# Performance work log

Hardware: AMD Instinct MI355X
Metric: run time of the kernel (lower is better)

The kernel has to match this reference:

```python
import jax, jax.numpy as jnp
import numpy as np

B, T, C, H = 2, 2048, 1024, 16
D = C // H  # head dim = 64

def setup_inputs() -> dict:
    key = jax.random.key(0)
    k1, k2, k3 = jax.random.split(key, 3)
    x = jax.random.normal(k1, (B, T, C), dtype=jnp.float32)
    w_attn = jax.random.normal(k2, (C, 3 * C), dtype=jnp.float32) * (1.0 / np.sqrt(C))
    w_proj = jax.random.normal(k3, (C, C), dtype=jnp.float32) * (1.0 / np.sqrt(C))
    return {"x": x, "w_attn": w_attn, "w_proj": w_proj}

def reference(x, w_attn, w_proj):
    # qkv projection: [B,T,3C]
    qkv = jnp.einsum('btc,cd->btd', x, w_attn)
    q, k, v = jnp.split(qkv, 3, axis=-1)
    # reshape to [B,H,T,D]
    q = q.reshape(B, T, H, D).transpose(0, 2, 1, 3)
    k = k.reshape(B, T, H, D).transpose(0, 2, 1, 3)
    v = v.reshape(B, T, H, D).transpose(0, 2, 1, 3)
    scale = 1.0 / jnp.sqrt(jnp.asarray(D, dtype=q.dtype))
    att = jnp.einsum('bhqd,bhkd->bhqk', q, k) * scale  # [B,H,T,T]
    att = jax.nn.softmax(att, axis=-1)
    y = jnp.einsum('bhqk,bhkd->bhqd', att, v)  # [B,H,T,D]
    y = y.transpose(0, 2, 1, 3).reshape(B, T, C)
    return jnp.einsum('btc,cd->btd', y, w_proj)
```

## Files before the change

### kernel.cpp

```cpp
#include <hip/hip_runtime.h>
#include <hip/hip_bf16.h>


typedef unsigned short u16;
using bf16x8 = __attribute__((ext_vector_type(8))) short;
using f32x4  = __attribute__((ext_vector_type(4))) float;

#define T_SEQ 2048
#define CDIM  1024

#define QSCALE 0.18033688011112042f

#if __has_builtin(__builtin_amdgcn_exp2f)
#define EXP2(x) __builtin_amdgcn_exp2f(x)
#else
#define EXP2(x) __expf((x) * 0.6931471805599453f)
#endif

__device__ inline u16 f2bf(float f) {
  __hip_bfloat16 h = __float2bfloat16(f);
  return *reinterpret_cast<u16*>(&h);
}
__device__ inline unsigned pk2bf(float a, float b) {
  return (unsigned)f2bf(a) | ((unsigned)f2bf(b) << 16);
}

__device__ inline void gload_lds16(const u16* g, u16* l) {
  __builtin_amdgcn_global_load_lds((const __attribute__((address_space(1))) void*)g,
                                   (__attribute__((address_space(3))) void*)l, 16, 0, 0);
}

__device__ inline int swz128(int r, int c) {
  return (((r << 7) + (c << 1)) ^ ((r & 7) << 4)) >> 1;
}

__global__ __launch_bounds__(256) void conv_bf16_kernel(const float* __restrict__ in,
                                                        u16* __restrict__ out, int n4) {
  int idx = blockIdx.x * 256 + threadIdx.x;
  if (idx >= n4) return;
  float4 v = reinterpret_cast<const float4*>(in)[idx];
  ushort4 o;
  o.x = f2bf(v.x); o.y = f2bf(v.y); o.z = f2bf(v.z); o.w = f2bf(v.w);
  reinterpret_cast<ushort4*>(out)[idx] = o;
}

__global__ __launch_bounds__(256) void transp_conv_kernel(const float* __restrict__ in,
                                                          u16* __restrict__ out, int R, int N,
                                                          int scale_rows, float scale) {
  __shared__ float tile[32][33];
  int nbx = N >> 5;
  int bx = blockIdx.x % nbx, by = blockIdx.x / nbx;
  int tx = threadIdx.x & 31, ty = threadIdx.x >> 5;
#pragma unroll
  for (int rr = ty; rr < 32; rr += 8)
    tile[rr][tx] = in[(long)(by * 32 + rr) * N + bx * 32 + tx];
  __syncthreads();
#pragma unroll
  for (int rr = ty; rr < 32; rr += 8) {
    float s = (bx * 32 + rr) < scale_rows ? scale : 1.0f;
    out[(long)(bx * 32 + rr) * R + by * 32 + tx] = f2bf(tile[tx][rr] * s);
  }
}

template <int MODE, int BN>
__global__ __launch_bounds__(256) void gemm_bt_kernel(const u16* __restrict__ A,
                                                      const u16* __restrict__ Bt,
                                                      void* __restrict__ C,
                                                      u16* __restrict__ vT,
                                                      int N, int K) {
  constexpr int NJ = BN / 32;
  constexpr int WN = BN / 2;
  __shared__ u16 As[2][128 * 32];
  __shared__ u16 Bs[2][BN * 32];
  const int tid = threadIdx.x;
  const int lane = tid & 63, wid = tid >> 6;
  const int l16 = lane & 15, lh = lane >> 4;
  const int wm = wid >> 1, wn = wid & 1;
  const int tm = blockIdx.x & 31;
  const int tn = blockIdx.x >> 5;

  f32x4 acc[4][NJ];
#pragma unroll
  for (int i = 0; i < 4; ++i)
#pragma unroll
    for (int j = 0; j < NJ; ++j)
      acc[i][j] = f32x4{0.f, 0.f, 0.f, 0.f};

  const long aRow = (long)(tm * 128 + wid * 16 + (lane >> 2)) * K + (lane & 3) * 8;
  const long bRow = (long)(tn * BN + wid * 16 + (lane >> 2)) * K + (lane & 3) * 8;
  const long rstep = (long)64 * K;
  const int ldsOff = wid * 512;

  gload_lds16(A + aRow, As[0] + ldsOff);
  gload_lds16(A + aRow + rstep, As[0] + ldsOff + 2048);
  gload_lds16(Bt + bRow, Bs[0] + ldsOff);
  if (BN == 128) gload_lds16(Bt + bRow + rstep, Bs[0] + ldsOff + 2048);
  __syncthreads();

  int cur = 0;
  for (int k0 = 0; k0 < K; k0 += 32) {
    if (k0 + 32 < K) {
      gload_lds16(A + aRow + k0 + 32, As[cur ^ 1] + ldsOff);
      gload_lds16(A + aRow + rstep + k0 + 32, As[cur ^ 1] + ldsOff + 2048);
      gload_lds16(Bt + bRow + k0 + 32, Bs[cur ^ 1] + ldsOff);
      if (BN == 128) gload_lds16(Bt + bRow + rstep + k0 + 32, Bs[cur ^ 1] + ldsOff + 2048);
    }
    bf16x8 af[4], bfr[NJ];
#pragma unroll
    for (int i = 0; i < 4; ++i)
      af[i] = *reinterpret_cast<const bf16x8*>(&As[cur][(wm * 64 + i * 16 + l16) * 32 + lh * 8]);
#pragma unroll
    for (int j = 0; j < NJ; ++j)
      bfr[j] = *reinterpret_cast<const bf16x8*>(&Bs[cur][(wn * WN + j * 16 + l16) * 32 + lh * 8]);
#pragma unroll
    for (int i = 0; i < 4; ++i)
#pragma unroll
      for (int j = 0; j < NJ; ++j)
        acc[i][j] = __builtin_amdgcn_mfma_f32_16x16x32_bf16(af[i], bfr[j], acc[i][j], 0, 0, 0);
    __syncthreads();
    cur ^= 1;
  }

  if (MODE == 2 && tn >= 16) {
    const int bsel = tm >> 4;
    const int t0 = (tm & 15) * 128 + wm * 64 + lh * 4;
#pragma unroll
    for (int i = 0; i < 4; ++i) {
#pragma unroll
      for (int j = 0; j < NJ; ++j) {
        const int h = 2 * (tn - 16) + wn;
        const int d = j * 16 + l16;
        u16* dst = vT + (long)((bsel * 16 + h) * 64 + d) * T_SEQ + t0 + i * 16;
        uint2 w2;
        w2.x = pk2bf(acc[i][j][0], acc[i][j][1]);
        w2.y = pk2bf(acc[i][j][2], acc[i][j][3]);
        *reinterpret_cast<uint2*>(dst) = w2;
      }
    }
    return;
  }

#pragma unroll
  for (int i = 0; i < 4; ++i) {
#pragma unroll
    for (int j = 0; j < NJ; ++j) {
#pragma unroll
      for (int r = 0; r < 4; ++r) {
        long row = tm * 128 + wm * 64 + i * 16 + lh * 4 + r;
        long col = tn * BN + wn * WN + j * 16 + l16;
        if (MODE == 1)
          reinterpret_cast<float*>(C)[row * N + col] = acc[i][j][r];
        else
          reinterpret_cast<u16*>(C)[row * N + col] = f2bf(acc[i][j][r]);
      }
    }
  }
}

__global__ __launch_bounds__(256) void vtrans_kernel(const u16* __restrict__ qkv,
                                                     u16* __restrict__ vT) {
  __shared__ u16 Ts[64 * 64];
  const int tid = threadIdx.x;
  const int bid = blockIdx.x;
  const int tt = bid & 31, bh = bid >> 5;
  const int b = bh >> 4, h = bh & 15;
  const int sr = tid >> 2, sc = (tid & 3) * 16;
  const u16* src = qkv + (long)(b * T_SEQ + tt * 64 + sr) * 3072 + 2 * CDIM + h * 64 + sc;
  uint4 v0 = *reinterpret_cast<const uint4*>(src);
  uint4 v1 = *reinterpret_cast<const uint4*>(src + 8);
  *reinterpret_cast<uint4*>(&Ts[swz128(sr, sc)]) = v0;
  *reinterpret_cast<uint4*>(&Ts[swz128(sr, sc + 8)]) = v1;
  __syncthreads();
  union { uint4 u[2]; u16 s[16]; } o;
#pragma unroll
  for (int i = 0; i < 16; ++i) o.s[i] = Ts[swz128(sc + i, sr)];
  u16* dst = vT + (long)(bh * 64 + sr) * T_SEQ + tt * 64 + sc;
  reinterpret_cast<uint4*>(dst)[0] = o.u[0];
  reinterpret_cast<uint4*>(dst)[1] = o.u[1];
}

__global__ __launch_bounds__(256) void attn_kernel(const u16* __restrict__ qkv,
                                                   const u16* __restrict__ vT,
                                                   u16* __restrict__ y) {
  __shared__ u16 Qs[64 * 64];
  __shared__ u16 Ks[64 * 64];
  __shared__ u16 Vt[64 * 64];
  __shared__ u16 Ps[4][16 * 64];
  const int tid = threadIdx.x;
  const int lane = tid & 63, wid = tid >> 6;
  const int l16 = lane & 15, lh = lane >> 4;
  const int bid = blockIdx.x;
  const int qt = bid & 31, h = (bid >> 5) & 15, b = bid >> 9;

  const u16* qbase = qkv + (long)(b * T_SEQ + qt * 64) * 3072 + h * 64;
  const u16* kbase = qkv + (long)(b * T_SEQ) * 3072 + CDIM + h * 64;
  const u16* vtbase = vT + (long)((b * 16 + h) * 64) * T_SEQ;

  const int sr = tid >> 2, sc = (tid & 3) * 16;
  const int ss0 = swz128(sr, sc), ss1 = swz128(sr, sc + 8);

  int kvo[2][4];
#pragma unroll
  for (int cb = 0; cb < 4; ++cb) {
    kvo[0][cb] = swz128(cb * 16 + l16, lh * 8);
    kvo[1][cb] = swz128(cb * 16 + l16, 32 + lh * 8);
  }
  const int pxor = (l16 & 7) << 3;
  int pwi[4];
#pragma unroll
  for (int cb = 0; cb < 4; ++cb) pwi[cb] = (l16 * 64 + cb * 16 + lh * 4) ^ pxor;
  const int pri0 = (l16 * 64 + lh * 8) ^ pxor;
  const int pri1 = (l16 * 64 + 32 + lh * 8) ^ pxor;

  {
    uint4 v0 = *reinterpret_cast<const uint4*>(qbase + (long)sr * 3072 + sc);
    uint4 v1 = *reinterpret_cast<const uint4*>(qbase + (long)sr * 3072 + sc + 8);
    *reinterpret_cast<uint4*>(&Qs[ss0]) = v0;
    *reinterpret_cast<uint4*>(&Qs[ss1]) = v1;
  }
  uint4 kr0 = *reinterpret_cast<const uint4*>(kbase + (long)sr * 3072 + sc);
  uint4 kr1 = *reinterpret_cast<const uint4*>(kbase + (long)sr * 3072 + sc + 8);
  uint4 vr0 = *reinterpret_cast<const uint4*>(vtbase + (long)sr * T_SEQ + sc);
  uint4 vr1 = *reinterpret_cast<const uint4*>(vtbase + (long)sr * T_SEQ + sc + 8);

  __syncthreads();
  bf16x8 qf0 = *reinterpret_cast<const bf16x8*>(&Qs[swz128(wid * 16 + l16, lh * 8)]);
  bf16x8 qf1 = *reinterpret_cast<const bf16x8*>(&Qs[swz128(wid * 16 + l16, 32 + lh * 8)]);

  f32x4 oacc[4];
  float lp = 0.f;
#pragma unroll
  for (int cb = 0; cb < 4; ++cb) oacc[cb] = f32x4{0.f, 0.f, 0.f, 0.f};

  for (int kt = 0; kt < 32; ++kt) {
    *reinterpret_cast<uint4*>(&Ks[ss0]) = kr0;
    *reinterpret_cast<uint4*>(&Ks[ss1]) = kr1;
    *reinterpret_cast<uint4*>(&Vt[ss0]) = vr0;
    *reinterpret_cast<uint4*>(&Vt[ss1]) = vr1;
    __syncthreads();
    if (kt < 31) {
      const u16* ks = kbase + (long)((kt + 1) * 64 + sr) * 3072 + sc;
      const u16* vs = vtbase + (long)sr * T_SEQ + (kt + 1) * 64 + sc;
      kr0 = *reinterpret_cast<const uint4*>(ks);
      kr1 = *reinterpret_cast<const uint4*>(ks + 8);
      vr0 = *reinterpret_cast<const uint4*>(vs);
      vr1 = *reinterpret_cast<const uint4*>(vs + 8);
    }

    f32x4 sacc[4];
#pragma unroll
    for (int cb = 0; cb < 4; ++cb) {
      sacc[cb] = f32x4{0.f, 0.f, 0.f, 0.f};
      bf16x8 kf0 = *reinterpret_cast<const bf16x8*>(&Ks[kvo[0][cb]]);
      bf16x8 kf1 = *reinterpret_cast<const bf16x8*>(&Ks[kvo[1][cb]]);
      sacc[cb] = __builtin_amdgcn_mfma_f32_16x16x32_bf16(kf0, qf0, sacc[cb], 0, 0, 0);
      sacc[cb] = __builtin_amdgcn_mfma_f32_16x16x32_bf16(kf1, qf1, sacc[cb], 0, 0, 0);
    }

    float p[4][4];
#pragma unroll
    for (int cb = 0; cb < 4; ++cb)
#pragma unroll
      for (int r = 0; r < 4; ++r) p[cb][r] = EXP2(sacc[cb][r]);
#pragma unroll
    for (int cb = 0; cb < 4; ++cb)
      lp += (p[cb][0] + p[cb][1]) + (p[cb][2] + p[cb][3]);
#pragma unroll
    for (int cb = 0; cb < 4; ++cb) {
      uint2 w2;
      w2.x = pk2bf(p[cb][0], p[cb][1]);
      w2.y = pk2bf(p[cb][2], p[cb][3]);
      *reinterpret_cast<uint2*>(&Ps[wid][pwi[cb]]) = w2;
    }

    bf16x8 pf0 = *reinterpret_cast<const bf16x8*>(&Ps[wid][pri0]);
    bf16x8 pf1 = *reinterpret_cast<const bf16x8*>(&Ps[wid][pri1]);

#pragma unroll
    for (int cb = 0; cb < 4; ++cb) {
      bf16x8 vf0 = *reinterpret_cast<const bf16x8*>(&Vt[kvo[0][cb]]);
      bf16x8 vf1 = *reinterpret_cast<const bf16x8*>(&Vt[kvo[1][cb]]);
      oacc[cb] = __builtin_amdgcn_mfma_f32_16x16x32_bf16(vf0, pf0, oacc[cb], 0, 0, 0);
      oacc[cb] = __builtin_amdgcn_mfma_f32_16x16x32_bf16(vf1, pf1, oacc[cb], 0, 0, 0);
    }
    __syncthreads();
  }

  float s = lp;
  s += __shfl_xor(s, 16);
  s += __shfl_xor(s, 32);
  const float inv = __builtin_amdgcn_rcpf(s);

#pragma unroll
  for (int cb = 0; cb < 4; ++cb) {
    uint2 w2;
    w2.x = pk2bf(oacc[cb][0] * inv, oacc[cb][1] * inv);
    w2.y = pk2bf(oacc[cb][2] * inv, oacc[cb][3] * inv);
    *reinterpret_cast<uint2*>(&Ps[wid][pwi[cb]]) = w2;
  }
  const int er = lane >> 2, ec = lane & 3;
  const int exr = (er & 7) << 3;
  const int eri0 = (er * 64 + ec * 16) ^ exr;
  const int eri1 = (er * 64 + ec * 16 + 8) ^ exr;
  uint4 o0 = *reinterpret_cast<const uint4*>(&Ps[wid][eri0]);
  uint4 o1 = *reinterpret_cast<const uint4*>(&Ps[wid][eri1]);
  u16* yrow = y + (long)(b * T_SEQ + qt * 64 + wid * 16 + er) * CDIM + h * 64 + ec * 16;
  reinterpret_cast<uint4*>(yrow)[0] = o0;
  *reinterpret_cast<uint4*>(yrow + 8) = o1;
}

extern "C" void kernel_launch(void* const* d_in, const int* in_sizes, int n_in,
                              void* d_out, int out_size, void* d_ws, size_t ws_size,
                              hipStream_t stream) {
  const float* x      = (const float*)d_in[0];
  const float* w_attn = (const float*)d_in[1];
  const float* w_proj = (const float*)d_in[2];

  char* ws = (char*)d_ws;
  u16* xb   = (u16*)(ws + 0);
  u16* wat  = (u16*)(ws + 8388608);
  u16* wpt  = (u16*)(ws + 14680064);
  u16* qkvb = (u16*)(ws + 16777216);
  u16* yb   = (u16*)(ws + 41943040);

  const bool fused = ws_size >= 58720256;
  u16* vT = fused ? (u16*)(ws + 50331648) : xb;

  conv_bf16_kernel<<<4096, 256, 0, stream>>>(x, xb, 1048576);
  transp_conv_kernel<<<96 * 32, 256, 0, stream>>>(w_attn, wat, 1024, 3072, 1024, QSCALE);
  transp_conv_kernel<<<32 * 32, 256, 0, stream>>>(w_proj, wpt, 1024, 1024, 0, 1.0f);
  if (fused) {
    gemm_bt_kernel<2, 128><<<32 * 24, 256, 0, stream>>>(xb, wat, qkvb, vT, 3072, 1024);
  } else {
    gemm_bt_kernel<0, 128><<<32 * 24, 256, 0, stream>>>(xb, wat, qkvb, nullptr, 3072, 1024);
    vtrans_kernel<<<32 * 32, 256, 0, stream>>>(qkvb, vT);
  }
  attn_kernel<<<2 * 16 * 32, 256, 0, stream>>>(qkvb, vT, yb);
  gemm_bt_kernel<1, 64><<<32 * 16, 256, 0, stream>>>(yb, wpt, d_out, nullptr, 1024, 1024);
}
```

Baseline: 196.6 us.

## Enlarge attention query tile to 128, double-buffer K/V via direct LDS loads

The attention kernel now handles 128 query rows per block, 32 per wave as two 16-row sub-blocks. This doubles the reuse of each K/V tile loaded into LDS and halves the total K/V traffic. K and V tiles are double-buffered and fetched with asynchronous global-to-LDS loads, replacing the register staging and the extra barrier per iteration. The output-projection GEMM swaps its MFMA operands so each lane can write float4 vectors instead of scalar floats. The trade-off is fewer blocks (512) and higher register and LDS use, which can lower occupancy.

```diff
diff --git a/kernel.cpp b/kernel.cpp
--- a/kernel.cpp
+++ b/kernel.cpp
@@ -115,10 +115,28 @@
 #pragma unroll
     for (int i = 0; i < 4; ++i)
 #pragma unroll
-      for (int j = 0; j < NJ; ++j)
-        acc[i][j] = __builtin_amdgcn_mfma_f32_16x16x32_bf16(af[i], bfr[j], acc[i][j], 0, 0, 0);
+      for (int j = 0; j < NJ; ++j) {
+        if (MODE == 1)
+          acc[i][j] = __builtin_amdgcn_mfma_f32_16x16x32_bf16(bfr[j], af[i], acc[i][j], 0, 0, 0);
+        else
+          acc[i][j] = __builtin_amdgcn_mfma_f32_16x16x32_bf16(af[i], bfr[j], acc[i][j], 0, 0, 0);
+      }
     __syncthreads();
     cur ^= 1;
+  }
+
+  if (MODE == 1) {
+#pragma unroll
+    for (int i = 0; i < 4; ++i) {
+#pragma unroll
+      for (int j = 0; j < NJ; ++j) {
+        long row = tm * 128 + wm * 64 + i * 16 + l16;
+        long col = tn * BN + wn * WN + j * 16 + lh * 4;
+        *reinterpret_cast<float4*>(reinterpret_cast<float*>(C) + row * N + col) =
+            float4{acc[i][j][0], acc[i][j][1], acc[i][j][2], acc[i][j][3]};
+      }
+    }
+    return;
   }
 
   if (MODE == 2 && tn >= 16) {
@@ -148,10 +166,7 @@
       for (int r = 0; r < 4; ++r) {
         long row = tm * 128 + wm * 64 + i * 16 + lh * 4 + r;
         long col = tn * BN + wn * WN + j * 16 + l16;
-        if (MODE == 1)
-          reinterpret_cast<float*>(C)[row * N + col] = acc[i][j][r];
-        else
-          reinterpret_cast<u16*>(C)[row * N + col] = f2bf(acc[i][j][r]);
+        reinterpret_cast<u16*>(C)[row * N + col] = f2bf(acc[i][j][r]);
       }
     }
   }
@@ -182,22 +197,45 @@
 __global__ __launch_bounds__(256) void attn_kernel(const u16* __restrict__ qkv,
                                                    const u16* __restrict__ vT,
                                                    u16* __restrict__ y) {
-  __shared__ u16 Qs[64 * 64];
-  __shared__ u16 Ks[64 * 64];
-  __shared__ u16 Vt[64 * 64];
-  __shared__ u16 Ps[4][16 * 64];
+  __shared__ u16 Qs[128 * 64];
+  __shared__ u16 Ks[2][64 * 64];
+  __shared__ u16 Vs[2][64 * 64];
+  __shared__ u16 Ps[4][32 * 64];
   const int tid = threadIdx.x;
   const int lane = tid & 63, wid = tid >> 6;
   const int l16 = lane & 15, lh = lane >> 4;
   const int bid = blockIdx.x;
-  const int qt = bid & 31, h = (bid >> 5) & 15, b = bid >> 9;
-
-  const u16* qbase = qkv + (long)(b * T_SEQ + qt * 64) * 3072 + h * 64;
+  const int qt = bid & 15, h = (bid >> 4) & 15, b = bid >> 8;
+
+  const u16* qbase = qkv + (long)(b * T_SEQ + qt * 128) * 3072 + h * 64;
   const u16* kbase = qkv + (long)(b * T_SEQ) * 3072 + CDIM + h * 64;
   const u16* vtbase = vT + (long)((b * 16 + h) * 64) * T_SEQ;
 
-  const int sr = tid >> 2, sc = (tid & 3) * 16;
-  const int ss0 = swz128(sr, sc), ss1 = swz128(sr, sc + 8);
+  const int srow = wid * 8 + (lane >> 3);
+  const int l8 = lane & 7;
+
+#pragma unroll
+  for (int q = 0; q < 4; ++q) {
+    int row = q * 32 + srow;
+    int colE = ((l8 ^ (row & 7)) << 3);
+    gload_lds16(qbase + (long)row * 3072 + colE, Qs + q * 2048 + wid * 512);
+  }
+#pragma unroll
+  for (int q = 0; q < 2; ++q) {
+    int row = q * 32 + srow;
+    int colE = ((l8 ^ (row & 7)) << 3);
+    gload_lds16(kbase + (long)row * 3072 + colE, Ks[0] + q * 2048 + wid * 512);
+    gload_lds16(vtbase + (long)row * T_SEQ + colE, Vs[0] + q * 2048 + wid * 512);
+  }
+  __syncthreads();
+
+  bf16x8 qf[2][2];
+#pragma unroll
+  for (int qb = 0; qb < 2; ++qb)
+#pragma unroll
+    for (int s = 0; s < 2; ++s)
+      qf[qb][s] = *reinterpret_cast<const bf16x8*>(
+          &Qs[swz128(wid * 32 + qb * 16 + l16, s * 32 + lh * 8)]);
 
   int kvo[2][4];
 #pragma unroll
@@ -205,108 +243,112 @@
     kvo[0][cb] = swz128(cb * 16 + l16, lh * 8);
     kvo[1][cb] = swz128(cb * 16 + l16, 32 + lh * 8);
   }
-  const int pxor = (l16 & 7) << 3;
-  int pwi[4];
-#pragma unroll
-  for (int cb = 0; cb < 4; ++cb) pwi[cb] = (l16 * 64 + cb * 16 + lh * 4) ^ pxor;
-  const int pri0 = (l16 * 64 + lh * 8) ^ pxor;
-  const int pri1 = (l16 * 64 + 32 + lh * 8) ^ pxor;
-
-  {
-    uint4 v0 = *reinterpret_cast<const uint4*>(qbase + (long)sr * 3072 + sc);
-    uint4 v1 = *reinterpret_cast<const uint4*>(qbase + (long)sr * 3072 + sc + 8);
-    *reinterpret_cast<uint4*>(&Qs[ss0]) = v0;
-    *reinterpret_cast<uint4*>(&Qs[ss1]) = v1;
-  }
-  uint4 kr0 = *reinterpret_cast<const uint4*>(kbase + (long)sr * 3072 + sc);
-  uint4 kr1 = *reinterpret_cast<const uint4*>(kbase + (long)sr * 3072 + sc + 8);
-  uint4 vr0 = *reinterpret_cast<const uint4*>(vtbase + (long)sr * T_SEQ + sc);
-  uint4 vr1 = *reinterpret_cast<const uint4*>(vtbase + (long)sr * T_SEQ + sc + 8);
-
-  __syncthreads();
-  bf16x8 qf0 = *reinterpret_cast<const bf16x8*>(&Qs[swz128(wid * 16 + l16, lh * 8)]);
-  bf16x8 qf1 = *reinterpret_cast<const bf16x8*>(&Qs[swz128(wid * 16 + l16, 32 + lh * 8)]);
-
-  f32x4 oacc[4];
-  float lp = 0.f;
-#pragma unroll
-  for (int cb = 0; cb < 4; ++cb) oacc[cb] = f32x4{0.f, 0.f, 0.f, 0.f};
-
+  int pwi[2][4], pri[2][2];
+#pragma unroll
+  for (int qb = 0; qb < 2; ++qb) {
+#pragma unroll
+    for (int cb = 0; cb < 4; ++cb) pwi[qb][cb] = swz128(qb * 16 + l16, cb * 16 + lh * 4);
+#pragma unroll
+    for (int s = 0; s < 2; ++s) pri[qb][s] = swz128(qb * 16 + l16, s * 32 + lh * 8);
+  }
+
+  f32x4 oacc[2][4];
+  float lp[2] = {0.f, 0.f};
+#pragma unroll
+  for (int qb = 0; qb < 2; ++qb)
+#pragma unroll
+    for (int cb = 0; cb < 4; ++cb) oacc[qb][cb] = f32x4{0.f, 0.f, 0.f, 0.f};
+
+  int cur = 0;
   for (int kt = 0; kt < 32; ++kt) {
-    *reinterpret_cast<uint4*>(&Ks[ss0]) = kr0;
-    *reinterpret_cast<uint4*>(&Ks[ss1]) = kr1;
-    *reinterpret_cast<uint4*>(&Vt[ss0]) = vr0;
-    *reinterpret_cast<uint4*>(&Vt[ss1]) = vr1;
+    if (kt < 31) {
+#pragma unroll
+      for (int q = 0; q < 2; ++q) {
+        int row = q * 32 + srow;
+        int colE = ((l8 ^ (row & 7)) << 3);
+        gload_lds16(kbase + (long)((kt + 1) * 64 + row) * 3072 + colE,
+                    Ks[cur ^ 1] + q * 2048 + wid * 512);
+        gload_lds16(vtbase + (long)row * T_SEQ + (kt + 1) * 64 + colE,
+                    Vs[cur ^ 1] + q * 2048 + wid * 512);
+      }
+    }
+
+    f32x4 sacc[2][4];
+#pragma unroll
+    for (int qb = 0; qb < 2; ++qb)
+#pragma unroll
+      for (int cb = 0; cb < 4; ++cb) sacc[qb][cb] = f32x4{0.f, 0.f, 0.f, 0.f};
+#pragma unroll
+    for (int cb = 0; cb < 4; ++cb) {
+      bf16x8 kf0 = *reinterpret_cast<const bf16x8*>(&Ks[cur][kvo[0][cb]]);
+      bf16x8 kf1 = *reinterpret_cast<const bf16x8*>(&Ks[cur][kvo[1][cb]]);
+#pragma unroll
+      for (int qb = 0; qb < 2; ++qb) {
+        sacc[qb][cb] = __builtin_amdgcn_mfma_f32_16x16x32_bf16(kf0, qf[qb][0], sacc[qb][cb], 0, 0, 0);
+        sacc[qb][cb] = __builtin_amdgcn_mfma_f32_16x16x32_bf16(kf1, qf[qb][1], sacc[qb][cb], 0, 0, 0);
+      }
+    }
+
+#pragma unroll
+    for (int qb = 0; qb < 2; ++qb) {
+#pragma unroll
+      for (int cb = 0; cb < 4; ++cb) {
+        float p0 = EXP2(sacc[qb][cb][0]), p1 = EXP2(sacc[qb][cb][1]);
+        float p2 = EXP2(sacc[qb][cb][2]), p3 = EXP2(sacc[qb][cb][3]);
+        lp[qb] += (p0 + p1) + (p2 + p3);
+        uint2 w2;
+        w2.x = pk2bf(p0, p1);
+        w2.y = pk2bf(p2, p3);
+        *reinterpret_cast<uint2*>(&Ps[wid][pwi[qb][cb]]) = w2;
+      }
+    }
+
+    bf16x8 pf[2][2];
+#pragma unroll
+    for (int qb = 0; qb < 2; ++qb)
+#pragma unroll
+      for (int s = 0; s < 2; ++s)
+        pf[qb][s] = *reinterpret_cast<const bf16x8*>(&Ps[wid][pri[qb][s]]);
+#pragma unroll
+    for (int cb = 0; cb < 4; ++cb) {
+      bf16x8 vf0 = *reinterpret_cast<const bf16x8*>(&Vs[cur][kvo[0][cb]]);
+      bf16x8 vf1 = *reinterpret_cast<const bf16x8*>(&Vs[cur][kvo[1][cb]]);
+#pragma unroll
+      for (int qb = 0; qb < 2; ++qb) {
+        oacc[qb][cb] = __builtin_amdgcn_mfma_f32_16x16x32_bf16(vf0, pf[qb][0], oacc[qb][cb], 0, 0, 0);
+        oacc[qb][cb] = __builtin_amdgcn_mfma_f32_16x16x32_bf16(vf1, pf[qb][1], oacc[qb][cb], 0, 0, 0);
+      }
+    }
     __syncthreads();
-    if (kt < 31) {
-      const u16* ks = kbase + (long)((kt + 1) * 64 + sr) * 3072 + sc;
-      const u16* vs = vtbase + (long)sr * T_SEQ + (kt + 1) * 64 + sc;
-      kr0 = *reinterpret_cast<const uint4*>(ks);
-      kr1 = *reinterpret_cast<const uint4*>(ks + 8);
-      vr0 = *reinterpret_cast<const uint4*>(vs);
-      vr1 = *reinterpret_cast<const uint4*>(vs + 8);
-    }
-
-    f32x4 sacc[4];
-#pragma unroll
-    for (int cb = 0; cb < 4; ++cb) {
-      sacc[cb] = f32x4{0.f, 0.f, 0.f, 0.f};
-      bf16x8 kf0 = *reinterpret_cast<const bf16x8*>(&Ks[kvo[0][cb]]);
-      bf16x8 kf1 = *reinterpret_cast<const bf16x8*>(&Ks[kvo[1][cb]]);
-      sacc[cb] = __builtin_amdgcn_mfma_f32_16x16x32_bf16(kf0, qf0, sacc[cb], 0, 0, 0);
-      sacc[cb] = __builtin_amdgcn_mfma_f32_16x16x32_bf16(kf1, qf1, sacc[cb], 0, 0, 0);
-    }
-
-    float p[4][4];
-#pragma unroll
-    for (int cb = 0; cb < 4; ++cb)
-#pragma unroll
-      for (int r = 0; r < 4; ++r) p[cb][r] = EXP2(sacc[cb][r]);
-#pragma unroll
-    for (int cb = 0; cb < 4; ++cb)
-      lp += (p[cb][0] + p[cb][1]) + (p[cb][2] + p[cb][3]);
+    cur ^= 1;
+  }
+
+  float inv[2];
+#pragma unroll
+  for (int qb = 0; qb < 2; ++qb) {
+    float s = lp[qb];
+    s += __shfl_xor(s, 16);
+    s += __shfl_xor(s, 32);
+    inv[qb] = __builtin_amdgcn_rcpf(s);
+  }
+
+#pragma unroll
+  for (int qb = 0; qb < 2; ++qb) {
 #pragma unroll
     for (int cb = 0; cb < 4; ++cb) {
       uint2 w2;
-      w2.x = pk2bf(p[cb][0], p[cb][1]);
-      w2.y = pk2bf(p[cb][2], p[cb][3]);
-      *reinterpret_cast<uint2*>(&Ps[wid][pwi[cb]]) = w2;
-    }
-
-    bf16x8 pf0 = *reinterpret_cast<const bf16x8*>(&Ps[wid][pri0]);
-    bf16x8 pf1 = *reinterpret_cast<const bf16x8*>(&Ps[wid][pri1]);
-
-#pragma unroll
-    for (int cb = 0; cb < 4; ++cb) {
-      bf16x8 vf0 = *reinterpret_cast<const bf16x8*>(&Vt[kvo[0][cb]]);
-      bf16x8 vf1 = *reinterpret_cast<const bf16x8*>(&Vt[kvo[1][cb]]);
-      oacc[cb] = __builtin_amdgcn_mfma_f32_16x16x32_bf16(vf0, pf0, oacc[cb], 0, 0, 0);
-      oacc[cb] = __builtin_amdgcn_mfma_f32_16x16x32_bf16(vf1, pf1, oacc[cb], 0, 0, 0);
-    }
-    __syncthreads();
-  }
-
-  float s = lp;
-  s += __shfl_xor(s, 16);
-  s += __shfl_xor(s, 32);
-  const float inv = __builtin_amdgcn_rcpf(s);
-
-#pragma unroll
-  for (int cb = 0; cb < 4; ++cb) {
-    uint2 w2;
-    w2.x = pk2bf(oacc[cb][0] * inv, oacc[cb][1] * inv);
-    w2.y = pk2bf(oacc[cb][2] * inv, oacc[cb][3] * inv);
-    *reinterpret_cast<uint2*>(&Ps[wid][pwi[cb]]) = w2;
-  }
-  const int er = lane >> 2, ec = lane & 3;
-  const int exr = (er & 7) << 3;
-  const int eri0 = (er * 64 + ec * 16) ^ exr;
-  const int eri1 = (er * 64 + ec * 16 + 8) ^ exr;
-  uint4 o0 = *reinterpret_cast<const uint4*>(&Ps[wid][eri0]);
-  uint4 o1 = *reinterpret_cast<const uint4*>(&Ps[wid][eri1]);
-  u16* yrow = y + (long)(b * T_SEQ + qt * 64 + wid * 16 + er) * CDIM + h * 64 + ec * 16;
-  reinterpret_cast<uint4*>(yrow)[0] = o0;
-  *reinterpret_cast<uint4*>(yrow + 8) = o1;
+      w2.x = pk2bf(oacc[qb][cb][0] * inv[qb], oacc[qb][cb][1] * inv[qb]);
+      w2.y = pk2bf(oacc[qb][cb][2] * inv[qb], oacc[qb][cb][3] * inv[qb]);
+      *reinterpret_cast<uint2*>(&Ps[wid][pwi[qb][cb]]) = w2;
+    }
+  }
+  const int er = lane >> 1, ec = (lane & 1) * 32;
+  u16* yrow = y + (long)(b * T_SEQ + qt * 128 + wid * 32 + er) * CDIM + h * 64 + ec;
+#pragma unroll
+  for (int k = 0; k < 4; ++k) {
+    uint4 o = *reinterpret_cast<const uint4*>(&Ps[wid][swz128(er, ec + k * 8)]);
+    *reinterpret_cast<uint4*>(yrow + k * 8) = o;
+  }
 }
 
 extern "C" void kernel_launch(void* const* d_in, const int* in_sizes, int n_in,
@@ -335,6 +377,6 @@
     gemm_bt_kernel<0, 128><<<32 * 24, 256, 0, stream>>>(xb, wat, qkvb, nullptr, 3072, 1024);
     vtrans_kernel<<<32 * 32, 256, 0, stream>>>(qkvb, vT);
   }
-  attn_kernel<<<2 * 16 * 32, 256, 0, stream>>>(qkvb, vT, yb);
+  attn_kernel<<<2 * 16 * 16, 256, 0, stream>>>(qkvb, vT, yb);
   gemm_bt_kernel<1, 64><<<32 * 16, 256, 0, stream>>>(yb, wpt, d_out, nullptr, 1024, 1024);
 }
```

After: 203.9 us. 1.04x slower.

## Split KV tile across waves in attention and vectorize fp32 projection stores

Applied to the files above, without the earlier changes.

The attention kernel now has each wave own a 16-key slice of every 64-key tile for all 64 queries, instead of one 16-query slice across all keys. The P matrix stays in registers and feeds a 16x16x16 MFMA directly, which removes the per-iteration LDS round trip for P. The cost is a cross-wave reduction at the end: partial outputs go through LDS as bf16, and row sums are combined in shared memory. The output-projection GEMM (MODE 1) swaps its MFMA operands so each lane writes a float4 instead of scalar stores.

```diff
diff --git a/kernel.cpp b/kernel.cpp
--- a/kernel.cpp
+++ b/kernel.cpp
@@ -4,6 +4,7 @@
 
 typedef unsigned short u16;
 using bf16x8 = __attribute__((ext_vector_type(8))) short;
+using bf16x4 = __attribute__((ext_vector_type(4))) short;
 using f32x4  = __attribute__((ext_vector_type(4))) float;
 
 #define T_SEQ 2048
@@ -23,6 +24,18 @@
 }
 __device__ inline unsigned pk2bf(float a, float b) {
   return (unsigned)f2bf(a) | ((unsigned)f2bf(b) << 16);
+}
+__device__ inline float bf2f(u16 v) { return __uint_as_float((unsigned)v << 16); }
+
+__device__ inline f32x4 mfma16(bf16x4 a, bf16x4 b, f32x4 c) {
+#if __has_builtin(__builtin_amdgcn_mfma_f32_16x16x16_bf16)
+  return __builtin_amdgcn_mfma_f32_16x16x16_bf16(a, b, c, 0, 0, 0);
+#elif __has_builtin(__builtin_amdgcn_mfma_f32_16x16x16bf16_1k)
+  return __builtin_amdgcn_mfma_f32_16x16x16bf16_1k(a, b, c, 0, 0, 0);
+#else
+  asm volatile("v_mfma_f32_16x16x16_bf16 %0, %1, %2, %0" : "+v"(c) : "v"(a), "v"(b));
+  return c;
+#endif
 }
 
 __device__ inline void gload_lds16(const u16* g, u16* l) {
@@ -115,10 +128,28 @@
 #pragma unroll
     for (int i = 0; i < 4; ++i)
 #pragma unroll
-      for (int j = 0; j < NJ; ++j)
-        acc[i][j] = __builtin_amdgcn_mfma_f32_16x16x32_bf16(af[i], bfr[j], acc[i][j], 0, 0, 0);
+      for (int j = 0; j < NJ; ++j) {
+        if (MODE == 1)
+          acc[i][j] = __builtin_amdgcn_mfma_f32_16x16x32_bf16(bfr[j], af[i], acc[i][j], 0, 0, 0);
+        else
+          acc[i][j] = __builtin_amdgcn_mfma_f32_16x16x32_bf16(af[i], bfr[j], acc[i][j], 0, 0, 0);
+      }
     __syncthreads();
     cur ^= 1;
+  }
+
+  if (MODE == 1) {
+#pragma unroll
+    for (int i = 0; i < 4; ++i) {
+#pragma unroll
+      for (int j = 0; j < NJ; ++j) {
+        long row = tm * 128 + wm * 64 + i * 16 + l16;
+        long col = tn * BN + wn * WN + j * 16 + lh * 4;
+        *reinterpret_cast<float4*>(reinterpret_cast<float*>(C) + row * N + col) =
+            float4{acc[i][j][0], acc[i][j][1], acc[i][j][2], acc[i][j][3]};
+      }
+    }
+    return;
   }
 
   if (MODE == 2 && tn >= 16) {
@@ -148,10 +179,7 @@
       for (int r = 0; r < 4; ++r) {
         long row = tm * 128 + wm * 64 + i * 16 + lh * 4 + r;
         long col = tn * BN + wn * WN + j * 16 + l16;
-        if (MODE == 1)
-          reinterpret_cast<float*>(C)[row * N + col] = acc[i][j][r];
-        else
-          reinterpret_cast<u16*>(C)[row * N + col] = f2bf(acc[i][j][r]);
+        reinterpret_cast<u16*>(C)[row * N + col] = f2bf(acc[i][j][r]);
       }
     }
   }
@@ -182,10 +210,13 @@
 __global__ __launch_bounds__(256) void attn_kernel(const u16* __restrict__ qkv,
                                                    const u16* __restrict__ vT,
                                                    u16* __restrict__ y) {
-  __shared__ u16 Qs[64 * 64];
-  __shared__ u16 Ks[64 * 64];
-  __shared__ u16 Vt[64 * 64];
-  __shared__ u16 Ps[4][16 * 64];
+  __shared__ char pool[33792];
+  u16* Qs = (u16*)pool;
+  u16* Ks = (u16*)(pool + 8192);
+  u16* Vs = (u16*)(pool + 16384);
+  u16* obuf = (u16*)pool;
+  float* rowsum = (float*)(pool + 32768);
+
   const int tid = threadIdx.x;
   const int lane = tid & 63, wid = tid >> 6;
   const int l16 = lane & 15, lh = lane >> 4;
@@ -199,18 +230,12 @@
   const int sr = tid >> 2, sc = (tid & 3) * 16;
   const int ss0 = swz128(sr, sc), ss1 = swz128(sr, sc + 8);
 
-  int kvo[2][4];
-#pragma unroll
-  for (int cb = 0; cb < 4; ++cb) {
-    kvo[0][cb] = swz128(cb * 16 + l16, lh * 8);
-    kvo[1][cb] = swz128(cb * 16 + l16, 32 + lh * 8);
-  }
-  const int pxor = (l16 & 7) << 3;
-  int pwi[4];
-#pragma unroll
-  for (int cb = 0; cb < 4; ++cb) pwi[cb] = (l16 * 64 + cb * 16 + lh * 4) ^ pxor;
-  const int pri0 = (l16 * 64 + lh * 8) ^ pxor;
-  const int pri1 = (l16 * 64 + 32 + lh * 8) ^ pxor;
+  int kfo[2];
+#pragma unroll
+  for (int s = 0; s < 2; ++s) kfo[s] = swz128(wid * 16 + l16, s * 32 + lh * 8);
+  int vfo[4];
+#pragma unroll
+  for (int db = 0; db < 4; ++db) vfo[db] = swz128(db * 16 + l16, wid * 16 + lh * 4);
 
   {
     uint4 v0 = *reinterpret_cast<const uint4*>(qbase + (long)sr * 3072 + sc);
@@ -224,19 +249,25 @@
   uint4 vr1 = *reinterpret_cast<const uint4*>(vtbase + (long)sr * T_SEQ + sc + 8);
 
   __syncthreads();
-  bf16x8 qf0 = *reinterpret_cast<const bf16x8*>(&Qs[swz128(wid * 16 + l16, lh * 8)]);
-  bf16x8 qf1 = *reinterpret_cast<const bf16x8*>(&Qs[swz128(wid * 16 + l16, 32 + lh * 8)]);
-
-  f32x4 oacc[4];
-  float lp = 0.f;
-#pragma unroll
-  for (int cb = 0; cb < 4; ++cb) oacc[cb] = f32x4{0.f, 0.f, 0.f, 0.f};
+  bf16x8 qf[4][2];
+#pragma unroll
+  for (int qb = 0; qb < 4; ++qb)
+#pragma unroll
+    for (int s = 0; s < 2; ++s)
+      qf[qb][s] = *reinterpret_cast<const bf16x8*>(&Qs[swz128(qb * 16 + l16, s * 32 + lh * 8)]);
+
+  f32x4 oacc[4][4];
+  float lp[4] = {0.f, 0.f, 0.f, 0.f};
+#pragma unroll
+  for (int db = 0; db < 4; ++db)
+#pragma unroll
+    for (int qb = 0; qb < 4; ++qb) oacc[db][qb] = f32x4{0.f, 0.f, 0.f, 0.f};
 
   for (int kt = 0; kt < 32; ++kt) {
     *reinterpret_cast<uint4*>(&Ks[ss0]) = kr0;
     *reinterpret_cast<uint4*>(&Ks[ss1]) = kr1;
-    *reinterpret_cast<uint4*>(&Vt[ss0]) = vr0;
-    *reinterpret_cast<uint4*>(&Vt[ss1]) = vr1;
+    *reinterpret_cast<uint4*>(&Vs[ss0]) = vr0;
+    *reinterpret_cast<uint4*>(&Vs[ss1]) = vr1;
     __syncthreads();
     if (kt < 31) {
       const u16* ks = kbase + (long)((kt + 1) * 64 + sr) * 3072 + sc;
@@ -247,66 +278,89 @@
       vr1 = *reinterpret_cast<const uint4*>(vs + 8);
     }
 
+    bf16x8 kf0 = *reinterpret_cast<const bf16x8*>(&Ks[kfo[0]]);
+    bf16x8 kf1 = *reinterpret_cast<const bf16x8*>(&Ks[kfo[1]]);
     f32x4 sacc[4];
 #pragma unroll
-    for (int cb = 0; cb < 4; ++cb) {
-      sacc[cb] = f32x4{0.f, 0.f, 0.f, 0.f};
-      bf16x8 kf0 = *reinterpret_cast<const bf16x8*>(&Ks[kvo[0][cb]]);
-      bf16x8 kf1 = *reinterpret_cast<const bf16x8*>(&Ks[kvo[1][cb]]);
-      sacc[cb] = __builtin_amdgcn_mfma_f32_16x16x32_bf16(kf0, qf0, sacc[cb], 0, 0, 0);
-      sacc[cb] = __builtin_amdgcn_mfma_f32_16x16x32_bf16(kf1, qf1, sacc[cb], 0, 0, 0);
-    }
-
-    float p[4][4];
-#pragma unroll
-    for (int cb = 0; cb < 4; ++cb)
-#pragma unroll
-      for (int r = 0; r < 4; ++r) p[cb][r] = EXP2(sacc[cb][r]);
-#pragma unroll
-    for (int cb = 0; cb < 4; ++cb)
-      lp += (p[cb][0] + p[cb][1]) + (p[cb][2] + p[cb][3]);
-#pragma unroll
-    for (int cb = 0; cb < 4; ++cb) {
+    for (int qb = 0; qb < 4; ++qb) {
+      sacc[qb] = f32x4{0.f, 0.f, 0.f, 0.f};
+      sacc[qb] = __builtin_amdgcn_mfma_f32_16x16x32_bf16(kf0, qf[qb][0], sacc[qb], 0, 0, 0);
+      sacc[qb] = __builtin_amdgcn_mfma_f32_16x16x32_bf16(kf1, qf[qb][1], sacc[qb], 0, 0, 0);
+    }
+
+    bf16x4 pf[4];
+#pragma unroll
+    for (int qb = 0; qb < 4; ++qb) {
+      float p0 = EXP2(sacc[qb][0]), p1 = EXP2(sacc[qb][1]);
+      float p2 = EXP2(sacc[qb][2]), p3 = EXP2(sacc[qb][3]);
+      lp[qb] += (p0 + p1) + (p2 + p3);
+      union { unsigned u[2]; bf16x4 v; } pu;
+      pu.u[0] = pk2bf(p0, p1);
+      pu.u[1] = pk2bf(p2, p3);
+      pf[qb] = pu.v;
+    }
+
+    bf16x4 vf[4];
+#pragma unroll
+    for (int db = 0; db < 4; ++db)
+      vf[db] = *reinterpret_cast<const bf16x4*>(&Vs[vfo[db]]);
+
+#pragma unroll
+    for (int db = 0; db < 4; ++db)
+#pragma unroll
+      for (int qb = 0; qb < 4; ++qb)
+        oacc[db][qb] = mfma16(vf[db], pf[qb], oacc[db][qb]);
+    __syncthreads();
+  }
+
+#pragma unroll
+  for (int qb = 0; qb < 4; ++qb) {
+    float s = lp[qb];
+    s += __shfl_xor(s, 16);
+    s += __shfl_xor(s, 32);
+    if (lane < 16) rowsum[wid * 64 + qb * 16 + lane] = s;
+  }
+
+  u16* ob = obuf + wid * 4096;
+#pragma unroll
+  for (int db = 0; db < 4; ++db) {
+#pragma unroll
+    for (int qb = 0; qb < 4; ++qb) {
       uint2 w2;
-      w2.x = pk2bf(p[cb][0], p[cb][1]);
-      w2.y = pk2bf(p[cb][2], p[cb][3]);
-      *reinterpret_cast<uint2*>(&Ps[wid][pwi[cb]]) = w2;
-    }
-
-    bf16x8 pf0 = *reinterpret_cast<const bf16x8*>(&Ps[wid][pri0]);
-    bf16x8 pf1 = *reinterpret_cast<const bf16x8*>(&Ps[wid][pri1]);
-
-#pragma unroll
-    for (int cb = 0; cb < 4; ++cb) {
-      bf16x8 vf0 = *reinterpret_cast<const bf16x8*>(&Vt[kvo[0][cb]]);
-      bf16x8 vf1 = *reinterpret_cast<const bf16x8*>(&Vt[kvo[1][cb]]);
-      oacc[cb] = __builtin_amdgcn_mfma_f32_16x16x32_bf16(vf0, pf0, oacc[cb], 0, 0, 0);
-      oacc[cb] = __builtin_amdgcn_mfma_f32_16x16x32_bf16(vf1, pf1, oacc[cb], 0, 0, 0);
-    }
-    __syncthreads();
-  }
-
-  float s = lp;
-  s += __shfl_xor(s, 16);
-  s += __shfl_xor(s, 32);
-  const float inv = __builtin_amdgcn_rcpf(s);
-
-#pragma unroll
-  for (int cb = 0; cb < 4; ++cb) {
-    uint2 w2;
-    w2.x = pk2bf(oacc[cb][0] * inv, oacc[cb][1] * inv);
-    w2.y = pk2bf(oacc[cb][2] * inv, oacc[cb][3] * inv);
-    *reinterpret_cast<uint2*>(&Ps[wid][pwi[cb]]) = w2;
-  }
-  const int er = lane >> 2, ec = lane & 3;
-  const int exr = (er & 7) << 3;
-  const int eri0 = (er * 64 + ec * 16) ^ exr;
-  const int eri1 = (er * 64 + ec * 16 + 8) ^ exr;
-  uint4 o0 = *reinterpret_cast<const uint4*>(&Ps[wid][eri0]);
-  uint4 o1 = *reinterpret_cast<const uint4*>(&Ps[wid][eri1]);
-  u16* yrow = y + (long)(b * T_SEQ + qt * 64 + wid * 16 + er) * CDIM + h * 64 + ec * 16;
-  reinterpret_cast<uint4*>(yrow)[0] = o0;
-  *reinterpret_cast<uint4*>(yrow + 8) = o1;
+      w2.x = pk2bf(oacc[db][qb][0], oacc[db][qb][1]);
+      w2.y = pk2bf(oacc[db][qb][2], oacc[db][qb][3]);
+      *reinterpret_cast<uint2*>(&ob[swz128(qb * 16 + l16, db * 16 + lh * 4)]) = w2;
+    }
+  }
+  __syncthreads();
+
+  {
+    const int q = tid >> 2, dch = (tid & 3) * 16;
+    const float inv = __builtin_amdgcn_rcpf(rowsum[q] + rowsum[64 + q] +
+                                            rowsum[128 + q] + rowsum[192 + q]);
+    float a[16];
+#pragma unroll
+    for (int j = 0; j < 16; ++j) a[j] = 0.f;
+    const int ri0 = swz128(q, dch), ri1 = swz128(q, dch + 8);
+#pragma unroll
+    for (int w = 0; w < 4; ++w) {
+      const u16* obw = obuf + w * 4096;
+      union { uint4 u; u16 s[8]; } r0, r1;
+      r0.u = *reinterpret_cast<const uint4*>(&obw[ri0]);
+      r1.u = *reinterpret_cast<const uint4*>(&obw[ri1]);
+#pragma unroll
+      for (int j = 0; j < 8; ++j) {
+        a[j] += bf2f(r0.s[j]);
+        a[8 + j] += bf2f(r1.s[j]);
+      }
+    }
+    union { uint4 u[2]; u16 s[16]; } o;
+#pragma unroll
+    for (int j = 0; j < 16; ++j) o.s[j] = f2bf(a[j] * inv);
+    u16* yrow = y + (long)(b * T_SEQ + qt * 64 + q) * CDIM + h * 64 + dch;
+    *reinterpret_cast<uint4*>(yrow) = o.u[0];
+    *reinterpret_cast<uint4*>(yrow + 8) = o.u[1];
+  }
 }
 
 extern "C" void kernel_launch(void* const* d_in, const int* in_sizes, int n_in,
```

Result: slower. 207.1 us (+5.3%).
